# Optimization experiments

Hardware: AMD Instinct MI355X
Metric: run time of the kernel (lower is better)

The kernel has to match this reference:

```python
import math
import jax, jax.numpy as jnp
import numpy as np


def setup_inputs() -> dict:
    key = jax.random.key(0)
    k1, k2 = jax.random.split(key)
    B, Sq, Sk, H, Hkv, D = 2, 2048, 2048, 16, 8, 128
    q = jax.random.normal(k1, (B, Sq, H, D), dtype=jnp.float32)
    kv = jax.random.normal(k2, (B, Sk, 2, Hkv, D), dtype=jnp.float32)
    return {"q": q, "kv": kv}


def reference(q, kv):
    # q: [B, Sq, H, D]; kv: [B, Sk, 2, Hkv, D]
    B, Sq, H, D = q.shape
    Sk = kv.shape[1]
    Hkv = kv.shape[3]
    if Hkv != H:
        # GQA: repeat each kv head g times consecutively ('... hkv d -> ... (hkv g) d')
        kv = jnp.repeat(kv, H // Hkv, axis=3)
    k = kv[:, :, 0]  # [B, Sk, H, D]
    v = kv[:, :, 1]  # [B, Sk, H, D]
    q = q.astype(jnp.float32)
    k = k.astype(jnp.float32)
    scale = 1.0 / math.sqrt(D)
    # scores: [B, H, Sq, Sk]
    scores = jnp.einsum('bqhd,bkhd->bhqk', q, k * scale)
    # causal mask with right-alignment offset: mask where col > row + Sk - Sq
    rows = jnp.arange(Sq)[:, None]
    cols = jnp.arange(Sk)[None, :]
    causal_mask = cols > rows + (Sk - Sq)  # [Sq, Sk]
    scores = jnp.where(causal_mask[None, None], jnp.float32(-10000.0), scores)
    attention = jax.nn.softmax(scores, axis=-1).astype(v.dtype)
    # output: [B, Sq, H, D]
    out = jnp.einsum('bhqk,bkhd->bqhd', attention, v)
    return out
```

## Files before the change

kernel.cpp:

```cpp
#include <hip/hip_runtime.h>
#include <stdint.h>


#define SQ 2048
#define SK 2048
#define NH 16
#define NKV 8
#define DH 128
#define KVSTRIDE (2*NKV*DH)
#define SCALE_LOG2E 0.12751743f

typedef __attribute__((ext_vector_type(8))) short bf8;
typedef __attribute__((ext_vector_type(4))) float f4;

__device__ __forceinline__ float fast_exp2(float x) {
  return __builtin_amdgcn_exp2f(x);
}

__device__ __forceinline__ short f2bf(float f) {
  uint32_t u = __builtin_bit_cast(uint32_t, f);
  u += 0x7FFFu + ((u >> 16) & 1u);
  return (short)(u >> 16);
}

__device__ __forceinline__ bf8 pack8(f4 a, f4 b) {
  bf8 v;
  v[0] = f2bf(a[0]); v[1] = f2bf(a[1]); v[2] = f2bf(a[2]); v[3] = f2bf(a[3]);
  v[4] = f2bf(b[0]); v[5] = f2bf(b[1]); v[6] = f2bf(b[2]); v[7] = f2bf(b[3]);
  return v;
}
__device__ __forceinline__ bf8 pack8s(f4 a, f4 b, float s) {
  bf8 v;
  v[0] = f2bf(a[0]*s); v[1] = f2bf(a[1]*s); v[2] = f2bf(a[2]*s); v[3] = f2bf(a[3]*s);
  v[4] = f2bf(b[0]*s); v[5] = f2bf(b[1]*s); v[6] = f2bf(b[2]*s); v[7] = f2bf(b[3]*s);
  return v;
}

template<int CTRL>
__device__ __forceinline__ float dppmov(float x) {
  int xi = __builtin_bit_cast(int, x);
  int r = __builtin_amdgcn_update_dpp(xi, xi, CTRL, 0xF, 0xF, false);
  return __builtin_bit_cast(float, r);
}
__device__ __forceinline__ float rowsum16(float v) {
  v += dppmov<0x121>(v);
  v += dppmov<0x122>(v);
  v += dppmov<0x124>(v);
  v += dppmov<0x128>(v);
  return v;
}
__device__ __forceinline__ float rowmax16(float v) {
  v = fmaxf(v, dppmov<0x121>(v));
  v = fmaxf(v, dppmov<0x122>(v));
  v = fmaxf(v, dppmov<0x124>(v));
  v = fmaxf(v, dppmov<0x128>(v));
  return v;
}

__device__ __forceinline__ void g2l16(const short* g, short* l) {
  __builtin_amdgcn_global_load_lds(
      (const __attribute__((address_space(1))) uint32_t*)g,
      (__attribute__((address_space(3))) uint32_t*)l, 16, 0, 0);
}

__global__ void conv_kv(const float* __restrict__ kv,
                        short* __restrict__ Kb, short* __restrict__ Vb) {
  int id = blockIdx.x * 256 + threadIdx.x;
  if (blockIdx.y == 0) {
    int c   = id & 15;
    int key = (id >> 4) & 63;
    int kt  = (id >> 10) & 31;
    int hk  = (id >> 15) & 7;
    int b   = (id >> 18) & 1;
    const float* src = kv + ((size_t)(b * SK + kt * 64 + key) * 2) * (NKV * DH)
                          + hk * DH + c * 8;
    f4 a = *(const f4*)src;
    f4 bb = *(const f4*)(src + 4);
    short* dst = Kb + ((size_t)((b * 8 + hk) * 32 + kt)) * 8192;
    *(bf8*)&dst[(key * 16 + (c ^ (key & 7))) * 8] = pack8(a, bb);
  } else {
    int d  = id & 127;
    int c  = (id >> 7) & 7;
    int kt = (id >> 10) & 31;
    int hk = (id >> 15) & 7;
    int b  = (id >> 18) & 1;
    const float* src = kv + ((size_t)(b * SK + kt * 64 + c * 8) * 2 + 1) * (NKV * DH)
                          + hk * DH + d;
    bf8 v;
#pragma unroll
    for (int kk = 0; kk < 8; ++kk) v[kk] = f2bf(src[(size_t)kk * KVSTRIDE]);
    short* dst = Vb + ((size_t)((b * 8 + hk) * 32 + kt)) * 8192;
    *(bf8*)&dst[(d * 8 + (c ^ (d & 7))) * 8] = v;
  }
}

__launch_bounds__(512, 2)
__global__ void fa_fwd3(const float* __restrict__ q,
                        const short* __restrict__ Kb,
                        const short* __restrict__ Vb,
                        float* __restrict__ out) {
  __shared__ __align__(16) short lsK[2][8192];
  __shared__ __align__(16) short lsV[2][8192];
  __shared__ __align__(16) short lsP[8][1536];

  const int tid  = threadIdx.x;
  const int w    = tid >> 6;
  const int l    = tid & 63;
  const int l15  = l & 15;
  const int quad = l >> 4;

  const int bx  = blockIdx.x;
  const int p   = bx >> 4;
  const int bhk = bx & 15;
  const int b   = bhk >> 3;
  const int hk  = bhk & 7;
  const int head  = hk * 2 + (w >> 2);
  const int rbase = (w & 3) * 16;

  const short* ktiles = Kb + ((size_t)((b * 8 + hk) * 32)) * 8192;
  const short* vtiles = Vb + ((size_t)((b * 8 + hk) * 32)) * 8192;
  short* myP = lsP[w];

  auto stage = [&](int kt, int nb) {
    const short* ks = ktiles + (size_t)kt * 8192 + tid * 8;
    const short* vs = vtiles + (size_t)kt * 8192 + tid * 8;
#pragma unroll
    for (int i = 0; i < 2; ++i) {
      g2l16(ks + i * 4096, &lsK[nb][i * 4096 + tid * 8]);
      g2l16(vs + i * 4096, &lsV[nb][i * 4096 + tid * 8]);
    }
  };

#pragma unroll 1
  for (int phase = 0; phase < 2; ++phase) {
    const int qt = phase ? (31 - p) : p;
    const int q0 = qt * 64;

    bf8 qf[4];
    {
      int row = q0 + rbase + l15;
      const float* qr = q + ((size_t)(b * SQ + row) * NH + head) * DH;
#pragma unroll
      for (int kc = 0; kc < 4; ++kc) {
        const float* src = qr + kc * 32 + quad * 8;
        f4 a = *(const f4*)src;
        f4 c = *(const f4*)(src + 4);
        qf[kc] = pack8s(a, c, SCALE_LOG2E);
      }
    }

    f4 O[8];
#pragma unroll
    for (int nt = 0; nt < 8; ++nt) O[nt] = (f4){0.f, 0.f, 0.f, 0.f};
    float lpart[4] = {0.f, 0.f, 0.f, 0.f};

    if (phase) __syncthreads();
    stage(0, 0);

    for (int kt = 0; kt <= qt; ++kt) {
      const int cur = kt & 1;
      __syncthreads();
      if (kt < qt) stage(kt + 1, cur ^ 1);

      f4 S[4];
#pragma unroll
      for (int nt = 0; nt < 4; ++nt) S[nt] = (f4){0.f, 0.f, 0.f, 0.f};
#pragma unroll
      for (int kc = 0; kc < 4; ++kc) {
#pragma unroll
        for (int nt = 0; nt < 4; ++nt) {
          int key = nt * 16 + l15;
          int c   = kc * 4 + quad;
          bf8 kf = *(const bf8*)&lsK[cur][(key * 16 + (c ^ (key & 7))) * 8];
          S[nt] = __builtin_amdgcn_mfma_f32_16x16x32_bf16(qf[kc], kf, S[nt], 0, 0, 0);
        }
      }

      if (kt == qt) {
#pragma unroll
        for (int nt = 0; nt < 4; ++nt)
#pragma unroll
          for (int r = 0; r < 4; ++r) {
            int rloc = rbase + quad * 4 + r;
            int kloc = nt * 16 + l15;
            if (kloc > rloc) S[nt][r] = -1e30f;
          }
      }

#pragma unroll
      for (int nt = 0; nt < 4; ++nt)
#pragma unroll
        for (int r = 0; r < 4; ++r) {
          float pe = fast_exp2(S[nt][r]);
          S[nt][r] = pe;
          lpart[r] += pe;
        }

#pragma unroll
      for (int r = 0; r < 4; ++r) {
        int m = quad * 4 + r;
#pragma unroll
        for (int nt = 0; nt < 4; ++nt) {
          int key = nt * 16 + l15;
          myP[(m * 8 + ((key >> 3) ^ (m & 7))) * 8 + (key & 7)] = f2bf(S[nt][r]);
        }
      }

#pragma unroll
      for (int kc = 0; kc < 2; ++kc) {
        int c = kc * 4 + quad;
        bf8 pf = *(const bf8*)&myP[(l15 * 8 + (c ^ (l15 & 7))) * 8];
#pragma unroll
        for (int nt = 0; nt < 8; ++nt) {
          int d = nt * 16 + l15;
          bf8 vf = *(const bf8*)&lsV[cur][(d * 8 + (c ^ (d & 7))) * 8];
          O[nt] = __builtin_amdgcn_mfma_f32_16x16x32_bf16(pf, vf, O[nt], 0, 0, 0);
        }
      }
    }

#pragma unroll
    for (int r = 0; r < 4; ++r) {
      float linv = 1.0f / rowsum16(lpart[r]);
      int row = q0 + rbase + quad * 4 + r;
      float* dst = out + ((size_t)(b * SQ + row) * NH + head) * DH + l15;
#pragma unroll
      for (int nt = 0; nt < 8; ++nt) dst[nt * 16] = O[nt][r] * linv;
    }
  }
}

__launch_bounds__(256, 2)
__global__ void fa_fwd_v1(const float* __restrict__ q,
                          const float* __restrict__ kv,
                          float* __restrict__ out) {
  __shared__ __align__(16) short lsK[64 * 128];
  __shared__ __align__(16) short lsV[128 * 64];
  __shared__ __align__(16) short lsP[4][32 * 64];

  const int tid  = threadIdx.x;
  const int w    = tid >> 6;
  const int l    = tid & 63;
  const int l15  = l & 15;
  const int quad = l >> 4;

  const int bx  = blockIdx.x;
  const int qt  = 31 - (bx >> 4);
  const int bhk = bx & 15;
  const int b   = bhk >> 3;
  const int hk  = bhk & 7;
  const int head  = hk * 2 + (w >> 1);
  const int mrow0 = (w & 1) * 32;
  const int q0    = qt * 64;

  const float* kbase = kv + (size_t)b * SK * KVSTRIDE + (size_t)hk * DH;
  const float* vbase = kbase + NKV * DH;

  bf8 qf[2][4];
#pragma unroll
  for (int mt = 0; mt < 2; ++mt)
#pragma unroll
    for (int kc = 0; kc < 4; ++kc) {
      int row = q0 + mrow0 + mt * 16 + l15;
      int d0  = kc * 32 + quad * 8;
      const float* src = q + ((size_t)(b * SQ + row) * NH + head) * DH + d0;
      f4 a = *(const f4*)src;
      f4 c = *(const f4*)(src + 4);
      qf[mt][kc] = pack8s(a, c, SCALE_LOG2E);
    }

  f4 O[2][8];
  float mrow[2][4], lrow[2][4];
#pragma unroll
  for (int mt = 0; mt < 2; ++mt) {
#pragma unroll
    for (int nt = 0; nt < 8; ++nt) O[mt][nt] = (f4){0.f, 0.f, 0.f, 0.f};
#pragma unroll
    for (int r = 0; r < 4; ++r) { mrow[mt][r] = -1e30f; lrow[mt][r] = 0.f; }
  }

  for (int kt = 0; kt <= qt; ++kt) {
    if (kt) __syncthreads();
    const int k0 = kt * 64;
#pragma unroll
    for (int i = 0; i < 4; ++i) {
      int id  = i * 256 + tid;
      int key = id >> 4;
      int c   = id & 15;
      const float* src = kbase + (size_t)(k0 + key) * KVSTRIDE + c * 8;
      f4 a = *(const f4*)src;
      f4 bb = *(const f4*)(src + 4);
      *(bf8*)&lsK[(key * 16 + (c ^ (key & 7))) * 8] = pack8(a, bb);
    }
#pragma unroll
    for (int i = 0; i < 4; ++i) {
      int u  = i * 4 + w;
      int kg = u >> 1;
      int d  = (u & 1) * 64 + l;
      const float* src = vbase + (size_t)(k0 + kg * 8) * KVSTRIDE + d;
      bf8 v;
#pragma unroll
      for (int kk = 0; kk < 8; ++kk) v[kk] = f2bf(src[(size_t)kk * KVSTRIDE]);
      *(bf8*)&lsV[(d * 8 + (kg ^ (d & 7))) * 8] = v;
    }
    __syncthreads();

    f4 S[2][4];
#pragma unroll
    for (int mt = 0; mt < 2; ++mt)
#pragma unroll
      for (int nt = 0; nt < 4; ++nt) S[mt][nt] = (f4){0.f, 0.f, 0.f, 0.f};
#pragma unroll
    for (int kc = 0; kc < 4; ++kc)
#pragma unroll
      for (int nt = 0; nt < 4; ++nt) {
        int key = nt * 16 + l15;
        int c   = kc * 4 + quad;
        bf8 kf = *(const bf8*)&lsK[(key * 16 + (c ^ (key & 7))) * 8];
        S[0][nt] = __builtin_amdgcn_mfma_f32_16x16x32_bf16(qf[0][kc], kf, S[0][nt], 0, 0, 0);
        S[1][nt] = __builtin_amdgcn_mfma_f32_16x16x32_bf16(qf[1][kc], kf, S[1][nt], 0, 0, 0);
      }

    if (kt == qt) {
#pragma unroll
      for (int mt = 0; mt < 2; ++mt)
#pragma unroll
        for (int nt = 0; nt < 4; ++nt)
#pragma unroll
          for (int r = 0; r < 4; ++r) {
            int rloc = mrow0 + mt * 16 + quad * 4 + r;
            int kloc = nt * 16 + l15;
            if (kloc > rloc) S[mt][nt][r] = -1e30f;
          }
    }

#pragma unroll
    for (int mt = 0; mt < 2; ++mt)
#pragma unroll
      for (int r = 0; r < 4; ++r) {
        float mx = fmaxf(fmaxf(S[mt][0][r], S[mt][1][r]),
                         fmaxf(S[mt][2][r], S[mt][3][r]));
        mx = rowmax16(mx);
        float mold = mrow[mt][r];
        float mnew = fmaxf(mold, mx);
        float alpha = fast_exp2(mold - mnew);
        mrow[mt][r] = mnew;
        float rs = 0.f;
#pragma unroll
        for (int nt = 0; nt < 4; ++nt) {
          float pe = fast_exp2(S[mt][nt][r] - mnew);
          S[mt][nt][r] = pe;
          rs += pe;
        }
        rs = rowsum16(rs);
        lrow[mt][r] = lrow[mt][r] * alpha + rs;
#pragma unroll
        for (int nt = 0; nt < 8; ++nt) O[mt][nt][r] *= alpha;
        int m = mt * 16 + quad * 4 + r;
#pragma unroll
        for (int nt = 0; nt < 4; ++nt) {
          int key = nt * 16 + l15;
          lsP[w][(m * 8 + ((key >> 3) ^ (m & 7))) * 8 + (key & 7)] =
              f2bf(S[mt][nt][r]);
        }
      }

#pragma unroll
    for (int kc = 0; kc < 2; ++kc) {
      bf8 pf[2];
#pragma unroll
      for (int mt = 0; mt < 2; ++mt) {
        int m = mt * 16 + l15;
        int c = kc * 4 + quad;
        pf[mt] = *(const bf8*)&lsP[w][(m * 8 + (c ^ (m & 7))) * 8];
      }
#pragma unroll
      for (int nt = 0; nt < 8; ++nt) {
        int d = nt * 16 + l15;
        int c = kc * 4 + quad;
        bf8 vf = *(const bf8*)&lsV[(d * 8 + (c ^ (d & 7))) * 8];
        O[0][nt] = __builtin_amdgcn_mfma_f32_16x16x32_bf16(pf[0], vf, O[0][nt], 0, 0, 0);
        O[1][nt] = __builtin_amdgcn_mfma_f32_16x16x32_bf16(pf[1], vf, O[1][nt], 0, 0, 0);
      }
    }
  }

#pragma unroll
  for (int mt = 0; mt < 2; ++mt)
#pragma unroll
    for (int r = 0; r < 4; ++r) {
      float linv = 1.0f / lrow[mt][r];
      int row = q0 + mrow0 + mt * 16 + quad * 4 + r;
      float* dst = out + ((size_t)(b * SQ + row) * NH + head) * DH + l15;
#pragma unroll
      for (int nt = 0; nt < 8; ++nt) dst[nt * 16] = O[mt][nt][r] * linv;
    }
}

extern "C" void kernel_launch(void* const* d_in, const int* in_sizes, int n_in,
                              void* d_out, int out_size, void* d_ws, size_t ws_size,
                              hipStream_t stream) {
  const float* q  = (const float*)d_in[0];
  const float* kv = (const float*)d_in[1];
  float* out      = (float*)d_out;
  (void)in_sizes; (void)n_in; (void)out_size;

  const size_t kb_elems = (size_t)2 * 8 * 32 * 8192;
  const size_t need = 2 * kb_elems * sizeof(short);

  if (ws_size >= need) {
    short* Kb = (short*)d_ws;
    short* Vb = Kb + kb_elems;
    conv_kv<<<dim3(2048, 2), 256, 0, stream>>>(kv, Kb, Vb);
    fa_fwd3<<<dim3(256), dim3(512), 0, stream>>>(q, Kb, Vb, out);
  } else {
    fa_fwd_v1<<<dim3(512), dim3(256), 0, stream>>>(q, kv, out);
  }
}
```

Measured before the change: 155.6 us.

## Keep P in registers via transposed MFMA and co-schedule paired causal tiles

The attention kernel now computes S transposed (K as the A operand), so the softmax probabilities land in registers already shaped for the P·V MFMA (16x16x16 bf16). That removes the per-wave LDS round trip for P. Each wave now handles two 16-row M tiles for a single head, and the two paired causal query tiles run concurrently in the two halves of the block over one shared K/V stream, replacing two sequential phases. The trade-offs are more accumulator registers, idle warps on the short side once their tile is finished, and a launch that requests extra dynamic shared memory.

```diff
diff --git a/kernel.cpp b/kernel.cpp
--- a/kernel.cpp
+++ b/kernel.cpp
@@ -11,7 +11,14 @@
 #define SCALE_LOG2E 0.12751743f
 
 typedef __attribute__((ext_vector_type(8))) short bf8;
+typedef __attribute__((ext_vector_type(4))) short v4s;
 typedef __attribute__((ext_vector_type(4))) float f4;
+
+#if __has_builtin(__builtin_amdgcn_mfma_f32_16x16x16bf16_1k)
+#define HAVE_MFMA_K16 1
+#else
+#define HAVE_MFMA_K16 0
+#endif
 
 __device__ __forceinline__ float fast_exp2(float x) {
   return __builtin_amdgcn_exp2f(x);
@@ -95,13 +102,11 @@
 }
 
 __launch_bounds__(512, 2)
-__global__ void fa_fwd3(const float* __restrict__ q,
+__global__ void fa_fwd5(const float* __restrict__ q,
                         const short* __restrict__ Kb,
                         const short* __restrict__ Vb,
                         float* __restrict__ out) {
-  __shared__ __align__(16) short lsK[2][8192];
-  __shared__ __align__(16) short lsV[2][8192];
-  __shared__ __align__(16) short lsP[8][1536];
+  __shared__ __align__(16) short heap[4][8192];
 
   const int tid  = threadIdx.x;
   const int w    = tid >> 6;
@@ -109,123 +114,147 @@
   const int l15  = l & 15;
   const int quad = l >> 4;
 
-  const int bx  = blockIdx.x;
-  const int p   = bx >> 4;
-  const int bhk = bx & 15;
-  const int b   = bhk >> 3;
-  const int hk  = bhk & 7;
-  const int head  = hk * 2 + (w >> 2);
-  const int rbase = (w & 3) * 16;
+  const int bx   = blockIdx.x;
+  const int p    = bx >> 4;
+  const int bhk  = bx & 15;
+  const int b    = bhk >> 3;
+  const int hk   = bhk & 7;
+  const int side = w >> 2;
+  const int w2   = w & 3;
+  const int head  = hk * 2 + (w2 >> 1);
+  const int rbase = (w2 & 1) * 32;
+  const int myqt  = side ? (31 - p) : p;
+  const int kmax  = 31 - p;
+  const int q0    = myqt * 64;
 
   const short* ktiles = Kb + ((size_t)((b * 8 + hk) * 32)) * 8192;
   const short* vtiles = Vb + ((size_t)((b * 8 + hk) * 32)) * 8192;
-  short* myP = lsP[w];
+
+  bf8 qf[2][4];
+#pragma unroll
+  for (int mt = 0; mt < 2; ++mt) {
+    int row = q0 + rbase + mt * 16 + l15;
+    const float* qr = q + ((size_t)(b * SQ + row) * NH + head) * DH;
+#pragma unroll
+    for (int kc = 0; kc < 4; ++kc) {
+      const float* src = qr + kc * 32 + quad * 8;
+      f4 a = *(const f4*)src;
+      f4 c = *(const f4*)(src + 4);
+      qf[mt][kc] = pack8s(a, c, SCALE_LOG2E);
+    }
+  }
+
+  f4 O[2][8];
+#pragma unroll
+  for (int mt = 0; mt < 2; ++mt)
+#pragma unroll
+    for (int dt = 0; dt < 8; ++dt) O[mt][dt] = (f4){0.f, 0.f, 0.f, 0.f};
+  float lpart[2] = {0.f, 0.f};
 
   auto stage = [&](int kt, int nb) {
     const short* ks = ktiles + (size_t)kt * 8192 + tid * 8;
     const short* vs = vtiles + (size_t)kt * 8192 + tid * 8;
-#pragma unroll
-    for (int i = 0; i < 2; ++i) {
-      g2l16(ks + i * 4096, &lsK[nb][i * 4096 + tid * 8]);
-      g2l16(vs + i * 4096, &lsV[nb][i * 4096 + tid * 8]);
-    }
+    g2l16(ks,        &heap[nb][tid * 8]);
+    g2l16(ks + 4096, &heap[nb][4096 + tid * 8]);
+    g2l16(vs,        &heap[2 + nb][tid * 8]);
+    g2l16(vs + 4096, &heap[2 + nb][4096 + tid * 8]);
   };
 
-#pragma unroll 1
-  for (int phase = 0; phase < 2; ++phase) {
-    const int qt = phase ? (31 - p) : p;
-    const int q0 = qt * 64;
-
-    bf8 qf[4];
-    {
-      int row = q0 + rbase + l15;
-      const float* qr = q + ((size_t)(b * SQ + row) * NH + head) * DH;
-#pragma unroll
-      for (int kc = 0; kc < 4; ++kc) {
-        const float* src = qr + kc * 32 + quad * 8;
-        f4 a = *(const f4*)src;
-        f4 c = *(const f4*)(src + 4);
-        qf[kc] = pack8s(a, c, SCALE_LOG2E);
-      }
-    }
-
-    f4 O[8];
-#pragma unroll
-    for (int nt = 0; nt < 8; ++nt) O[nt] = (f4){0.f, 0.f, 0.f, 0.f};
-    float lpart[4] = {0.f, 0.f, 0.f, 0.f};
-
-    if (phase) __syncthreads();
-    stage(0, 0);
-
-    for (int kt = 0; kt <= qt; ++kt) {
-      const int cur = kt & 1;
-      __syncthreads();
-      if (kt < qt) stage(kt + 1, cur ^ 1);
-
-      f4 S[4];
-#pragma unroll
-      for (int nt = 0; nt < 4; ++nt) S[nt] = (f4){0.f, 0.f, 0.f, 0.f};
+  stage(0, 0);
+
+  for (int kt = 0; kt <= kmax; ++kt) {
+    const int cur = kt & 1;
+    __syncthreads();
+    if (kt < kmax) stage(kt + 1, cur ^ 1);
+
+    if (kt <= myqt) {
+      const short* lk = heap[cur];
+      const short* lv = heap[2 + cur];
+
+      f4 S[2][4];
+#pragma unroll
+      for (int mt = 0; mt < 2; ++mt)
+#pragma unroll
+        for (int nt = 0; nt < 4; ++nt) S[mt][nt] = (f4){0.f, 0.f, 0.f, 0.f};
 #pragma unroll
       for (int kc = 0; kc < 4; ++kc) {
 #pragma unroll
         for (int nt = 0; nt < 4; ++nt) {
           int key = nt * 16 + l15;
           int c   = kc * 4 + quad;
-          bf8 kf = *(const bf8*)&lsK[cur][(key * 16 + (c ^ (key & 7))) * 8];
-          S[nt] = __builtin_amdgcn_mfma_f32_16x16x32_bf16(qf[kc], kf, S[nt], 0, 0, 0);
+          bf8 kf = *(const bf8*)&lk[(key * 16 + (c ^ (key & 7))) * 8];
+          S[0][nt] = __builtin_amdgcn_mfma_f32_16x16x32_bf16(kf, qf[0][kc], S[0][nt], 0, 0, 0);
+          S[1][nt] = __builtin_amdgcn_mfma_f32_16x16x32_bf16(kf, qf[1][kc], S[1][nt], 0, 0, 0);
         }
       }
 
-      if (kt == qt) {
+      if (kt == myqt) {
 #pragma unroll
         for (int nt = 0; nt < 4; ++nt)
 #pragma unroll
           for (int r = 0; r < 4; ++r) {
-            int rloc = rbase + quad * 4 + r;
-            int kloc = nt * 16 + l15;
-            if (kloc > rloc) S[nt][r] = -1e30f;
+            int keyl = nt * 16 + quad * 4 + r;
+            if (keyl > rbase + l15)      S[0][nt][r] = -1e30f;
+            if (keyl > rbase + 16 + l15) S[1][nt][r] = -1e30f;
           }
       }
 
-#pragma unroll
-      for (int nt = 0; nt < 4; ++nt)
-#pragma unroll
-        for (int r = 0; r < 4; ++r) {
-          float pe = fast_exp2(S[nt][r]);
-          S[nt][r] = pe;
-          lpart[r] += pe;
+      v4s pf[2][4];
+#pragma unroll
+      for (int mt = 0; mt < 2; ++mt)
+#pragma unroll
+        for (int nt = 0; nt < 4; ++nt) {
+          f4 e;
+#pragma unroll
+          for (int r = 0; r < 4; ++r) {
+            e[r] = fast_exp2(S[mt][nt][r]);
+            lpart[mt] += e[r];
+          }
+          v4s pk;
+          pk[0] = f2bf(e[0]); pk[1] = f2bf(e[1]);
+          pk[2] = f2bf(e[2]); pk[3] = f2bf(e[3]);
+          pf[mt][nt] = pk;
         }
 
 #pragma unroll
-      for (int r = 0; r < 4; ++r) {
-        int m = quad * 4 + r;
-#pragma unroll
-        for (int nt = 0; nt < 4; ++nt) {
-          int key = nt * 16 + l15;
-          myP[(m * 8 + ((key >> 3) ^ (m & 7))) * 8 + (key & 7)] = f2bf(S[nt][r]);
+      for (int kt16 = 0; kt16 < 4; ++kt16) {
+#if !HAVE_MFMA_K16
+        bf8 p0z = (bf8){pf[0][kt16][0], pf[0][kt16][1], pf[0][kt16][2], pf[0][kt16][3], 0, 0, 0, 0};
+        bf8 p1z = (bf8){pf[1][kt16][0], pf[1][kt16][1], pf[1][kt16][2], pf[1][kt16][3], 0, 0, 0, 0};
+#endif
+#pragma unroll
+        for (int dt = 0; dt < 8; ++dt) {
+          int d = dt * 16 + l15;
+          int c = kt16 * 2 + (quad >> 1);
+          const short* vp = &lv[(d * 8 + (c ^ (d & 7))) * 8 + (quad & 1) * 4];
+          v4s vf = *(const v4s*)vp;
+#if HAVE_MFMA_K16
+          O[0][dt] = __builtin_amdgcn_mfma_f32_16x16x16bf16_1k(vf, pf[0][kt16], O[0][dt], 0, 0, 0);
+          O[1][dt] = __builtin_amdgcn_mfma_f32_16x16x16bf16_1k(vf, pf[1][kt16], O[1][dt], 0, 0, 0);
+#else
+          bf8 vz = (bf8){vf[0], vf[1], vf[2], vf[3], 0, 0, 0, 0};
+          O[0][dt] = __builtin_amdgcn_mfma_f32_16x16x32_bf16(vz, p0z, O[0][dt], 0, 0, 0);
+          O[1][dt] = __builtin_amdgcn_mfma_f32_16x16x32_bf16(vz, p1z, O[1][dt], 0, 0, 0);
+#endif
         }
       }
-
-#pragma unroll
-      for (int kc = 0; kc < 2; ++kc) {
-        int c = kc * 4 + quad;
-        bf8 pf = *(const bf8*)&myP[(l15 * 8 + (c ^ (l15 & 7))) * 8];
-#pragma unroll
-        for (int nt = 0; nt < 8; ++nt) {
-          int d = nt * 16 + l15;
-          bf8 vf = *(const bf8*)&lsV[cur][(d * 8 + (c ^ (d & 7))) * 8];
-          O[nt] = __builtin_amdgcn_mfma_f32_16x16x32_bf16(pf, vf, O[nt], 0, 0, 0);
-        }
-      }
-    }
-
-#pragma unroll
-    for (int r = 0; r < 4; ++r) {
-      float linv = 1.0f / rowsum16(lpart[r]);
-      int row = q0 + rbase + quad * 4 + r;
-      float* dst = out + ((size_t)(b * SQ + row) * NH + head) * DH + l15;
-#pragma unroll
-      for (int nt = 0; nt < 8; ++nt) dst[nt * 16] = O[nt][r] * linv;
+    }
+  }
+
+#pragma unroll
+  for (int mt = 0; mt < 2; ++mt) {
+    float lsum = lpart[mt];
+    lsum += __shfl_xor(lsum, 16, 64);
+    lsum += __shfl_xor(lsum, 32, 64);
+    float linv = 1.0f / lsum;
+    int row = q0 + rbase + mt * 16 + l15;
+    float* dst = out + ((size_t)(b * SQ + row) * NH + head) * DH + quad * 4;
+#pragma unroll
+    for (int dt = 0; dt < 8; ++dt) {
+      f4 v;
+      v[0] = O[mt][dt][0] * linv; v[1] = O[mt][dt][1] * linv;
+      v[2] = O[mt][dt][2] * linv; v[3] = O[mt][dt][3] * linv;
+      *(f4*)&dst[dt * 16] = v;
     }
   }
 }
@@ -412,7 +441,7 @@
     short* Kb = (short*)d_ws;
     short* Vb = Kb + kb_elems;
     conv_kv<<<dim3(2048, 2), 256, 0, stream>>>(kv, Kb, Vb);
-    fa_fwd3<<<dim3(256), dim3(512), 0, stream>>>(q, Kb, Vb, out);
+    fa_fwd5<<<dim3(256), dim3(512), 24576, stream>>>(q, Kb, Vb, out);
   } else {
     fa_fwd_v1<<<dim3(512), dim3(256), 0, stream>>>(q, kv, out);
   }
```

Result: slower. 161.4 us (+3.7%).

## Compute transposed scores to keep P in registers and read V from global

Applied to the files above, without the earlier changes.

The QK^T MFMA now swaps its operands so each lane holds S transposed. The exponentiated probabilities can then feed the PV MFMA directly as 16x16x16 bf16 operands, with no trip through LDS. V is no longer staged in shared memory: it is stored unswizzled in d-major layout by the conversion kernel and read straight from global/L2 in 4-element chunks. The row-sum reduction changes to cross-quad shuffles, and outputs are written as vectorized f4 stores. This removes the LDS P round-trip and V staging and cuts LDS use, but V loads now hit global memory uncoalesced-ish inside the inner loop, and the smaller MFMAs issue more instructions.

```diff
diff --git a/kernel.cpp b/kernel.cpp
--- a/kernel.cpp
+++ b/kernel.cpp
@@ -11,6 +11,7 @@
 #define SCALE_LOG2E 0.12751743f
 
 typedef __attribute__((ext_vector_type(8))) short bf8;
+typedef __attribute__((ext_vector_type(4))) short v4s;
 typedef __attribute__((ext_vector_type(4))) float f4;
 
 __device__ __forceinline__ float fast_exp2(float x) {
@@ -79,29 +80,27 @@
     short* dst = Kb + ((size_t)((b * 8 + hk) * 32 + kt)) * 8192;
     *(bf8*)&dst[(key * 16 + (c ^ (key & 7))) * 8] = pack8(a, bb);
   } else {
-    int d  = id & 127;
-    int c  = (id >> 7) & 7;
+    int c3 = id & 7;
+    int d  = (id >> 3) & 127;
     int kt = (id >> 10) & 31;
     int hk = (id >> 15) & 7;
     int b  = (id >> 18) & 1;
-    const float* src = kv + ((size_t)(b * SK + kt * 64 + c * 8) * 2 + 1) * (NKV * DH)
-                          + hk * DH + d;
+    const float* vsrc = kv + ((size_t)(b * SK + kt * 64 + c3 * 8) * 2 + 1) * (NKV * DH)
+                           + hk * DH + d;
     bf8 v;
 #pragma unroll
-    for (int kk = 0; kk < 8; ++kk) v[kk] = f2bf(src[(size_t)kk * KVSTRIDE]);
+    for (int kk = 0; kk < 8; ++kk) v[kk] = f2bf(vsrc[(size_t)kk * KVSTRIDE]);
     short* dst = Vb + ((size_t)((b * 8 + hk) * 32 + kt)) * 8192;
-    *(bf8*)&dst[(d * 8 + (c ^ (d & 7))) * 8] = v;
+    *(bf8*)&dst[d * 64 + c3 * 8] = v;
   }
 }
 
 __launch_bounds__(512, 2)
-__global__ void fa_fwd3(const float* __restrict__ q,
+__global__ void fa_fwd7(const float* __restrict__ q,
                         const short* __restrict__ Kb,
                         const short* __restrict__ Vb,
                         float* __restrict__ out) {
   __shared__ __align__(16) short lsK[2][8192];
-  __shared__ __align__(16) short lsV[2][8192];
-  __shared__ __align__(16) short lsP[8][1536];
 
   const int tid  = threadIdx.x;
   const int w    = tid >> 6;
@@ -110,7 +109,7 @@
   const int quad = l >> 4;
 
   const int bx  = blockIdx.x;
-  const int p   = bx >> 4;
+  const int px  = bx >> 4;
   const int bhk = bx & 15;
   const int b   = bhk >> 3;
   const int hk  = bhk & 7;
@@ -119,21 +118,16 @@
 
   const short* ktiles = Kb + ((size_t)((b * 8 + hk) * 32)) * 8192;
   const short* vtiles = Vb + ((size_t)((b * 8 + hk) * 32)) * 8192;
-  short* myP = lsP[w];
 
   auto stage = [&](int kt, int nb) {
     const short* ks = ktiles + (size_t)kt * 8192 + tid * 8;
-    const short* vs = vtiles + (size_t)kt * 8192 + tid * 8;
-#pragma unroll
-    for (int i = 0; i < 2; ++i) {
-      g2l16(ks + i * 4096, &lsK[nb][i * 4096 + tid * 8]);
-      g2l16(vs + i * 4096, &lsV[nb][i * 4096 + tid * 8]);
-    }
+    g2l16(ks,        &lsK[nb][tid * 8]);
+    g2l16(ks + 4096, &lsK[nb][4096 + tid * 8]);
   };
 
 #pragma unroll 1
   for (int phase = 0; phase < 2; ++phase) {
-    const int qt = phase ? (31 - p) : p;
+    const int qt = phase ? (31 - px) : px;
     const int q0 = qt * 64;
 
     bf8 qf[4];
@@ -151,8 +145,8 @@
 
     f4 O[8];
 #pragma unroll
-    for (int nt = 0; nt < 8; ++nt) O[nt] = (f4){0.f, 0.f, 0.f, 0.f};
-    float lpart[4] = {0.f, 0.f, 0.f, 0.f};
+    for (int dt = 0; dt < 8; ++dt) O[dt] = (f4){0.f, 0.f, 0.f, 0.f};
+    f4 lsum4 = (f4){0.f, 0.f, 0.f, 0.f};
 
     if (phase) __syncthreads();
     stage(0, 0);
@@ -162,6 +156,9 @@
       __syncthreads();
       if (kt < qt) stage(kt + 1, cur ^ 1);
 
+      const short* lk = lsK[cur];
+      const short* vt = vtiles + (size_t)kt * 8192;
+
       f4 S[4];
 #pragma unroll
       for (int nt = 0; nt < 4; ++nt) S[nt] = (f4){0.f, 0.f, 0.f, 0.f};
@@ -171,8 +168,8 @@
         for (int nt = 0; nt < 4; ++nt) {
           int key = nt * 16 + l15;
           int c   = kc * 4 + quad;
-          bf8 kf = *(const bf8*)&lsK[cur][(key * 16 + (c ^ (key & 7))) * 8];
-          S[nt] = __builtin_amdgcn_mfma_f32_16x16x32_bf16(qf[kc], kf, S[nt], 0, 0, 0);
+          bf8 kf = *(const bf8*)&lk[(key * 16 + (c ^ (key & 7))) * 8];
+          S[nt] = __builtin_amdgcn_mfma_f32_16x16x32_bf16(kf, qf[kc], S[nt], 0, 0, 0);
         }
       }
 
@@ -181,51 +178,51 @@
         for (int nt = 0; nt < 4; ++nt)
 #pragma unroll
           for (int r = 0; r < 4; ++r) {
-            int rloc = rbase + quad * 4 + r;
-            int kloc = nt * 16 + l15;
-            if (kloc > rloc) S[nt][r] = -1e30f;
+            int keyl = nt * 16 + quad * 4 + r;
+            if (keyl > rbase + l15) S[nt][r] = -1e30f;
           }
       }
 
-#pragma unroll
-      for (int nt = 0; nt < 4; ++nt)
-#pragma unroll
-        for (int r = 0; r < 4; ++r) {
-          float pe = fast_exp2(S[nt][r]);
-          S[nt][r] = pe;
-          lpart[r] += pe;
-        }
-
-#pragma unroll
-      for (int r = 0; r < 4; ++r) {
-        int m = quad * 4 + r;
-#pragma unroll
-        for (int nt = 0; nt < 4; ++nt) {
-          int key = nt * 16 + l15;
-          myP[(m * 8 + ((key >> 3) ^ (m & 7))) * 8 + (key & 7)] = f2bf(S[nt][r]);
-        }
-      }
-
-#pragma unroll
-      for (int kc = 0; kc < 2; ++kc) {
-        int c = kc * 4 + quad;
-        bf8 pf = *(const bf8*)&myP[(l15 * 8 + (c ^ (l15 & 7))) * 8];
-#pragma unroll
-        for (int nt = 0; nt < 8; ++nt) {
-          int d = nt * 16 + l15;
-          bf8 vf = *(const bf8*)&lsV[cur][(d * 8 + (c ^ (d & 7))) * 8];
-          O[nt] = __builtin_amdgcn_mfma_f32_16x16x32_bf16(pf, vf, O[nt], 0, 0, 0);
-        }
-      }
-    }
-
-#pragma unroll
-    for (int r = 0; r < 4; ++r) {
-      float linv = 1.0f / rowsum16(lpart[r]);
-      int row = q0 + rbase + quad * 4 + r;
-      float* dst = out + ((size_t)(b * SQ + row) * NH + head) * DH + l15;
-#pragma unroll
-      for (int nt = 0; nt < 8; ++nt) dst[nt * 16] = O[nt][r] * linv;
+      v4s pf[4];
+#pragma unroll
+      for (int nt = 0; nt < 4; ++nt) {
+        f4 e;
+#pragma unroll
+        for (int r = 0; r < 4; ++r) e[r] = fast_exp2(S[nt][r]);
+        lsum4 += e;
+        v4s pk;
+        pk[0] = f2bf(e[0]); pk[1] = f2bf(e[1]);
+        pk[2] = f2bf(e[2]); pk[3] = f2bf(e[3]);
+        pf[nt] = pk;
+      }
+
+#pragma unroll
+      for (int dt = 0; dt < 8; ++dt) {
+        int d = dt * 16 + l15;
+        const short* vrow = vt + d * 64 + quad * 4;
+        v4s vf0 = *(const v4s*)(vrow);
+        v4s vf1 = *(const v4s*)(vrow + 16);
+        v4s vf2 = *(const v4s*)(vrow + 32);
+        v4s vf3 = *(const v4s*)(vrow + 48);
+        O[dt] = __builtin_amdgcn_mfma_f32_16x16x16bf16_1k(vf0, pf[0], O[dt], 0, 0, 0);
+        O[dt] = __builtin_amdgcn_mfma_f32_16x16x16bf16_1k(vf1, pf[1], O[dt], 0, 0, 0);
+        O[dt] = __builtin_amdgcn_mfma_f32_16x16x16bf16_1k(vf2, pf[2], O[dt], 0, 0, 0);
+        O[dt] = __builtin_amdgcn_mfma_f32_16x16x16bf16_1k(vf3, pf[3], O[dt], 0, 0, 0);
+      }
+    }
+
+    float lsum = lsum4[0] + lsum4[1] + lsum4[2] + lsum4[3];
+    lsum += __shfl_xor(lsum, 16, 64);
+    lsum += __shfl_xor(lsum, 32, 64);
+    float linv = 1.0f / lsum;
+    int row = q0 + rbase + l15;
+    float* dst = out + ((size_t)(b * SQ + row) * NH + head) * DH + quad * 4;
+#pragma unroll
+    for (int dt = 0; dt < 8; ++dt) {
+      f4 v;
+      v[0] = O[dt][0] * linv; v[1] = O[dt][1] * linv;
+      v[2] = O[dt][2] * linv; v[3] = O[dt][3] * linv;
+      *(f4*)&dst[dt * 16] = v;
     }
   }
 }
@@ -412,7 +409,7 @@
     short* Kb = (short*)d_ws;
     short* Vb = Kb + kb_elems;
     conv_kv<<<dim3(2048, 2), 256, 0, stream>>>(kv, Kb, Vb);
-    fa_fwd3<<<dim3(256), dim3(512), 0, stream>>>(q, Kb, Vb, out);
+    fa_fwd7<<<dim3(256), dim3(512), 0, stream>>>(q, Kb, Vb, out);
   } else {
     fa_fwd_v1<<<dim3(512), dim3(256), 0, stream>>>(q, kv, out);
   }
```

Result: slower. 359.8 us (+131.2%).
